# Kernel optimization log

Hardware: AMD Instinct MI355X
Metric: run time of the kernel (lower is better)

## Reference

```python
import jax, jax.numpy as jnp
import numpy as np

EMBED_DIM = 16
HIDDEN = 256
MAX_ORDER = 6
N_EXPERTS = MAX_ORDER + 1
SIZES = [(2 ** (o + 1) + 1) ** 2 for o in range(N_EXPERTS)]  # maze pixels per order
S_MAX = SIZES[-1]  # 16641
D_IN = S_MAX + EMBED_DIM  # padded concat width; embed rows live at [S_MAX:]
BATCH = 1024


def setup_inputs() -> dict:
    key = jax.random.key(0)
    ks = jax.random.split(key, 12)
    w = 0.02  # weight init scale
    return {
        "mazes": jax.random.normal(ks[0], (BATCH, S_MAX), dtype=jnp.float32),
        "orders": jax.random.randint(ks[1], (BATCH,), 0, N_EXPERTS).astype(jnp.int32),
        "embed_table": jax.random.normal(ks[2], (N_EXPERTS, EMBED_DIM), dtype=jnp.float32),
        # per-order input layers, padded to a common [D_IN, 4H]; rows [size_o:S_MAX] unused for order o
        "W_in": jax.random.normal(ks[3], (N_EXPERTS, D_IN, 4 * HIDDEN), dtype=jnp.float32) * w,
        "b_in": jax.random.normal(ks[4], (N_EXPERTS, 4 * HIDDEN), dtype=jnp.float32) * w,
        "W1": jax.random.normal(ks[5], (4 * HIDDEN, 2 * HIDDEN), dtype=jnp.float32) * w,
        "b1": jax.random.normal(ks[6], (2 * HIDDEN,), dtype=jnp.float32) * w,
        "W2": jax.random.normal(ks[7], (2 * HIDDEN, HIDDEN), dtype=jnp.float32) * w,
        "b2": jax.random.normal(ks[8], (HIDDEN,), dtype=jnp.float32) * w,
        "W3": jax.random.normal(ks[9], (HIDDEN, 1), dtype=jnp.float32) * w,
        "b3": jax.random.normal(ks[10], (1,), dtype=jnp.float32) * w,
    }


def reference(mazes, orders, embed_table, W_in, b_in, W1, b1, W2, b2, W3, b3):
    # orders index the embedding table and select the per-order input layer
    e = embed_table[orders]  # [B, E]
    h = jnp.zeros((mazes.shape[0], 4 * HIDDEN), dtype=mazes.dtype)
    # fixed, small loop over experts (structurally distinct weight slices)
    for o in range(N_EXPERTS):
        s = SIZES[o]
        # concat([maze_flat[:s], embed]) exactly as torch.cat([maze_flat, embed])
        x = jnp.concatenate([mazes[:, :s], e], axis=1)  # [B, s+E]
        W = jnp.concatenate([W_in[o, :s], W_in[o, S_MAX:]], axis=0)  # [s+E, 4H]
        y = jax.nn.leaky_relu(x @ W + b_in[o], 0.2)  # [B, 4H]
        h = jnp.where((orders == o)[:, None], y, h)
    z = jax.nn.leaky_relu(h @ W1 + b1, 0.2)
    z = jax.nn.leaky_relu(z @ W2 + b2, 0.2)
    return jax.nn.sigmoid(z @ W3 + b3)  # [B, 1]
```

## Files before the change

kernel.cpp:

```cpp
#include <hip/hip_runtime.h>
#include <cstdint>
#include <cstddef>

#define NEXP 7
#define EMBED_DIM 16
#define FOURH 1024
#define TWOH 512
#define HID 256
#define S_MAX 16641
#define D_IN (S_MAX + EMBED_DIM)
#define BATCH 1024
#define MTILE 192
#define MROWS 384

__constant__ int d_SIZES[NEXP] = {9, 25, 81, 289, 1089, 4225, 16641};
__constant__ int d_KPAD[NEXP] = {64, 64, 128, 320, 1152, 4288, 16704};
__constant__ int d_AOFF[NEXP] = {0, 64, 128, 256, 576, 1728, 6016};
__constant__ int d_KCOFF[NEXP + 1] = {0, 1, 2, 3, 4, 7, 16, 49};

typedef short bf16x8 __attribute__((ext_vector_type(8)));
typedef float f32x4 __attribute__((ext_vector_type(4)));

__device__ __forceinline__ float lrelu(float x) { return x > 0.f ? x : 0.2f * x; }

__device__ __forceinline__ unsigned short f2bf(float x) {
  union { float f; unsigned u; } v;
  v.f = x;
  unsigned r = v.u + 0x7FFFu + ((v.u >> 16) & 1u);
  return (unsigned short)(r >> 16);
}

__global__ __launch_bounds__(1024) void bucket_kernel(
    const int* __restrict__ orders, int* __restrict__ counts,
    int* __restrict__ bases, int* __restrict__ list) {
  __shared__ int c[NEXP], p[NEXP];
  int t = threadIdx.x;
  if (t < NEXP) c[t] = 0;
  __syncthreads();
  int o = orders[t];
  atomicAdd(&c[o], 1);
  __syncthreads();
  if (t == 0) {
    int s = 0;
    for (int i = 0; i < NEXP; ++i) { p[i] = s; s += c[i]; }
  }
  __syncthreads();
  if (t < NEXP) { counts[t] = c[t]; bases[t] = p[t]; }
  __syncthreads();
  int pos = atomicAdd(&p[o], 1);
  list[pos] = t;
}

__global__ __launch_bounds__(1024) void hinit_kernel(
    const float* __restrict__ embed, const float* __restrict__ W_in,
    const float* __restrict__ b_in, float* __restrict__ hinit) {
  int o = blockIdx.x, j = threadIdx.x;
  float a = b_in[o * FOURH + j];
  const float* wr = W_in + (size_t)o * D_IN * FOURH + (size_t)S_MAX * FOURH + j;
#pragma unroll
  for (int e = 0; e < EMBED_DIM; ++e)
    a = fmaf(embed[o * EMBED_DIM + e], wr[(size_t)e * FOURH], a);
  hinit[o * FOURH + j] = a;
}

__global__ __launch_bounds__(256) void hb_kernel(
    const int* __restrict__ orders, const float* __restrict__ hinit,
    float* __restrict__ h) {
  int b = blockIdx.x;
  int o = orders[b];
  const float4* src = (const float4*)(hinit + (size_t)o * FOURH);
  float4* dst = (float4*)(h + (size_t)b * FOURH);
  dst[threadIdx.x] = src[threadIdx.x];
}

__global__ __launch_bounds__(256) void gather_kernel(
    const float* __restrict__ mazes, const int* __restrict__ counts,
    const int* __restrict__ bases, const int* __restrict__ list,
    unsigned short* __restrict__ Ab) {
  int o = blockIdx.x / MROWS;
  int m = blockIdx.x % MROWS;
  int n = counts[o];
  int so = d_SIZES[o];
  int Kp = d_KPAD[o];
  const float* src = nullptr;
  if (m < n) src = mazes + (size_t)list[bases[o] + m] * S_MAX;
  unsigned short* dst = Ab + (size_t)d_AOFF[o] * MROWS + (size_t)m * Kp;
  int nk8 = Kp >> 3;
  for (int k8 = threadIdx.x; k8 < nk8; k8 += 256) {
    int k = k8 * 8;
    union { unsigned short u[8]; uint4 v; } pk;
#pragma unroll
    for (int e = 0; e < 8; ++e) {
      float val = (src && (k + e) < so) ? src[k + e] : 0.f;
      pk.u[e] = f2bf(val);
    }
    *(uint4*)(dst + k) = pk.v;
  }
}

__global__ __launch_bounds__(256, 2) void layerin_mfma(
    const unsigned short* __restrict__ Ab, const float* __restrict__ W_in,
    const int* __restrict__ counts, const int* __restrict__ bases,
    const int* __restrict__ list, float* __restrict__ h) {
  int bx = blockIdx.x;
  int o = 0;
#pragma unroll
  for (int t = 1; t < NEXP; ++t)
    if (bx >= d_KCOFF[t]) o = t;
  int kc = bx - d_KCOFF[o];
  int n = counts[o];
  int m_base = blockIdx.z * MTILE;
  if (m_base >= n) return;

  __shared__ unsigned short sA[8 * 194 * 8];
  __shared__ int sid[MTILE];

  int tid = threadIdx.x;
  int wave = tid >> 6, lane = tid & 63;
  int q = lane >> 4, l16 = lane & 15;

  if (tid < MTILE) sid[tid] = (m_base + tid < n) ? list[bases[o] + m_base + tid] : 0;

  int so = d_SIZES[o];
  int Kp = d_KPAD[o];
  int klo = kc * 512;
  int klen = min(512, Kp - klo);

  int n0 = blockIdx.y * 128 + wave * 32;
  const float* Wc = W_in + (size_t)o * D_IN * FOURH + n0 + l16;
  const unsigned short* Abase =
      Ab + (size_t)d_AOFF[o] * MROWS + (size_t)m_base * Kp + klo;

  f32x4 acc[12][2];
#pragma unroll
  for (int mt = 0; mt < 12; ++mt) {
    acc[mt][0] = (f32x4)0.f;
    acc[mt][1] = (f32x4)0.f;
  }

  int kg = tid & 7;
  int mrow = tid >> 3;

  for (int ks = 0; ks < klen; ks += 64) {
    __syncthreads();
#pragma unroll
    for (int r = 0; r < 6; ++r) {
      int m = r * 32 + mrow;
      uint4 v = *(const uint4*)(Abase + (size_t)m * Kp + ks + kg * 8);
      *(uint4*)&sA[((kg * 194 + m) << 3)] = v;
    }
    __syncthreads();
#pragma unroll
    for (int st = 0; st < 2; ++st) {
      int kb = klo + ks + st * 32 + q * 8;
      bf16x8 bf0, bf1;
#pragma unroll
      for (int j = 0; j < 8; ++j) {
        int kj = kb + j;
        if (kj >= so) kj = so - 1;
        float w0 = Wc[(size_t)kj * FOURH];
        float w1 = Wc[(size_t)kj * FOURH + 16];
        bf0[j] = (short)f2bf(w0);
        bf1[j] = (short)f2bf(w1);
      }
#pragma unroll
      for (int mt = 0; mt < 12; ++mt) {
        bf16x8 af = *(const bf16x8*)&sA[(((st * 4 + q) * 194 + mt * 16 + l16) << 3)];
        acc[mt][0] = __builtin_amdgcn_mfma_f32_16x16x32_bf16(af, bf0, acc[mt][0], 0, 0, 0);
        acc[mt][1] = __builtin_amdgcn_mfma_f32_16x16x32_bf16(af, bf1, acc[mt][1], 0, 0, 0);
      }
    }
  }

  int colA = n0 + l16, colB = n0 + 16 + l16;
#pragma unroll
  for (int mt = 0; mt < 12; ++mt) {
#pragma unroll
    for (int r = 0; r < 4; ++r) {
      int m = mt * 16 + q * 4 + r;
      if (m_base + m < n) {
        int s = sid[m];
        atomicAdd(&h[(size_t)s * FOURH + colA], acc[mt][0][r]);
        atomicAdd(&h[(size_t)s * FOURH + colB], acc[mt][1][r]);
      }
    }
  }
}

template <int KD, int JD, bool ACT_IN>
__global__ __launch_bounds__(256) void mlp_kernel(
    const float* __restrict__ X, const float* __restrict__ W,
    const float* __restrict__ b, float* __restrict__ Y) {
  constexpr int MT2 = 8, KT2 = 256;
  __shared__ float sh[MT2][KT2];
  int tid = threadIdx.x;
  int j = blockIdx.x * 256 + tid;
  int m0 = blockIdx.y * MT2;
  int row = tid >> 5, u = tid & 31;
  const float* xp = X + (size_t)(m0 + row) * KD;
  float acc[MT2];
#pragma unroll
  for (int i = 0; i < MT2; ++i) acc[i] = 0.f;
  for (int kb0 = 0; kb0 < KD; kb0 += KT2) {
    __syncthreads();
#pragma unroll
    for (int c = 0; c < 2; ++c) {
      int kl = c * 128 + u * 4;
      float4 v = *(const float4*)(xp + kb0 + kl);
      if (ACT_IN) {
        v.x = lrelu(v.x); v.y = lrelu(v.y); v.z = lrelu(v.z); v.w = lrelu(v.w);
      }
      *(float4*)&sh[row][kl] = v;
    }
    __syncthreads();
    const float* wb = W + (size_t)kb0 * JD + j;
#pragma unroll 4
    for (int qq = 0; qq < KT2 / 4; ++qq) {
      float w0 = wb[(size_t)(qq * 4 + 0) * JD];
      float w1 = wb[(size_t)(qq * 4 + 1) * JD];
      float w2 = wb[(size_t)(qq * 4 + 2) * JD];
      float w3 = wb[(size_t)(qq * 4 + 3) * JD];
#pragma unroll
      for (int i = 0; i < MT2; ++i) {
        float4 m = *(const float4*)&sh[i][qq * 4];
        acc[i] = fmaf(m.x, w0, acc[i]);
        acc[i] = fmaf(m.y, w1, acc[i]);
        acc[i] = fmaf(m.z, w2, acc[i]);
        acc[i] = fmaf(m.w, w3, acc[i]);
      }
    }
  }
  float bb = b[j];
#pragma unroll
  for (int i = 0; i < MT2; ++i)
    Y[(size_t)(m0 + i) * JD + j] = lrelu(acc[i] + bb);
}

__global__ __launch_bounds__(256) void layer3_kernel(
    const float* __restrict__ z2, const float* __restrict__ W3,
    const float* __restrict__ b3, float* __restrict__ out) {
  int wave = threadIdx.x >> 6, lane = threadIdx.x & 63;
  int b = blockIdx.x * 4 + wave;
  float4 v = *(const float4*)&z2[(size_t)b * HID + lane * 4];
  float4 w = *(const float4*)&W3[lane * 4];
  float d = v.x * w.x + v.y * w.y + v.z * w.z + v.w * w.w;
#pragma unroll
  for (int off = 32; off; off >>= 1) d += __shfl_down(d, off);
  if (lane == 0) out[b] = 1.f / (1.f + expf(-(d + b3[0])));
}

extern "C" void kernel_launch(void* const* d_in, const int* in_sizes, int n_in,
                              void* d_out, int out_size, void* d_ws, size_t ws_size,
                              hipStream_t stream) {
  const float* mazes = (const float*)d_in[0];
  const int* orders = (const int*)d_in[1];
  const float* embed = (const float*)d_in[2];
  const float* W_in = (const float*)d_in[3];
  const float* b_in = (const float*)d_in[4];
  const float* W1 = (const float*)d_in[5];
  const float* b1 = (const float*)d_in[6];
  const float* W2 = (const float*)d_in[7];
  const float* b2 = (const float*)d_in[8];
  const float* W3 = (const float*)d_in[9];
  const float* b3 = (const float*)d_in[10];
  float* out = (float*)d_out;

  char* ws = (char*)d_ws;
  int* counts = (int*)ws;
  int* bases = counts + 8;
  int* list = counts + 16;
  float* hinit = (float*)(ws + 64 * 1024);
  float* h = (float*)(ws + 128 * 1024);
  float* z1 = (float*)(ws + 128 * 1024 + 4 * 1024 * 1024);
  unsigned short* Ab = (unsigned short*)(ws + 128 * 1024 + 8 * 1024 * 1024);
  float* z2 = h;

  bucket_kernel<<<1, 1024, 0, stream>>>(orders, counts, bases, list);
  hinit_kernel<<<NEXP, 1024, 0, stream>>>(embed, W_in, b_in, hinit);
  gather_kernel<<<NEXP * MROWS, 256, 0, stream>>>(mazes, counts, bases, list, Ab);
  hb_kernel<<<BATCH, 256, 0, stream>>>(orders, hinit, h);
  layerin_mfma<<<dim3(49, 8, 2), 256, 0, stream>>>(Ab, W_in, counts, bases, list, h);
  mlp_kernel<FOURH, TWOH, true><<<dim3(2, 128), 256, 0, stream>>>(h, W1, b1, z1);
  mlp_kernel<TWOH, HID, false><<<dim3(1, 128), 256, 0, stream>>>(z1, W2, b2, z2);
  layer3_kernel<<<256, 256, 0, stream>>>(z2, W3, b3, out);
}
```

Before: 804.9 us.

## Fuse small setup kernels and merge layer2 with final layer3 reduction

Merges bucketing and hinit into one prep kernel, folds the per-row h initialisation into the gather kernel, and fuses the second MLP layer with the final dot-product and sigmoid. The first MLP layer now has each thread compute two columns for four rows, using float2 weight loads. The main aim is to cut kernel launches and the z2 round trip through memory. In exchange, layer 2 runs on smaller 4-row tiles, which reuses each weight load less.

```diff
diff --git a/kernel.cpp b/kernel.cpp
--- a/kernel.cpp
+++ b/kernel.cpp
@@ -30,55 +30,55 @@
   return (unsigned short)(r >> 16);
 }
 
-__global__ __launch_bounds__(1024) void bucket_kernel(
+__global__ __launch_bounds__(1024) void prep_kernel(
     const int* __restrict__ orders, int* __restrict__ counts,
-    int* __restrict__ bases, int* __restrict__ list) {
+    int* __restrict__ bases, int* __restrict__ list,
+    const float* __restrict__ embed, const float* __restrict__ W_in,
+    const float* __restrict__ b_in, float* __restrict__ hinit) {
   __shared__ int c[NEXP], p[NEXP];
   int t = threadIdx.x;
-  if (t < NEXP) c[t] = 0;
-  __syncthreads();
-  int o = orders[t];
-  atomicAdd(&c[o], 1);
-  __syncthreads();
-  if (t == 0) {
-    int s = 0;
-    for (int i = 0; i < NEXP; ++i) { p[i] = s; s += c[i]; }
-  }
-  __syncthreads();
-  if (t < NEXP) { counts[t] = c[t]; bases[t] = p[t]; }
-  __syncthreads();
-  int pos = atomicAdd(&p[o], 1);
-  list[pos] = t;
-}
-
-__global__ __launch_bounds__(1024) void hinit_kernel(
-    const float* __restrict__ embed, const float* __restrict__ W_in,
-    const float* __restrict__ b_in, float* __restrict__ hinit) {
-  int o = blockIdx.x, j = threadIdx.x;
-  float a = b_in[o * FOURH + j];
-  const float* wr = W_in + (size_t)o * D_IN * FOURH + (size_t)S_MAX * FOURH + j;
-#pragma unroll
-  for (int e = 0; e < EMBED_DIM; ++e)
-    a = fmaf(embed[o * EMBED_DIM + e], wr[(size_t)e * FOURH], a);
-  hinit[o * FOURH + j] = a;
-}
-
-__global__ __launch_bounds__(256) void hb_kernel(
-    const int* __restrict__ orders, const float* __restrict__ hinit,
-    float* __restrict__ h) {
-  int b = blockIdx.x;
-  int o = orders[b];
-  const float4* src = (const float4*)(hinit + (size_t)o * FOURH);
-  float4* dst = (float4*)(h + (size_t)b * FOURH);
-  dst[threadIdx.x] = src[threadIdx.x];
-}
-
-__global__ __launch_bounds__(256) void gather_kernel(
+  if (blockIdx.x == 0) {
+    if (t < NEXP) c[t] = 0;
+    __syncthreads();
+    int o = orders[t];
+    atomicAdd(&c[o], 1);
+    __syncthreads();
+    if (t == 0) {
+      int s = 0;
+      for (int i = 0; i < NEXP; ++i) { p[i] = s; s += c[i]; }
+    }
+    __syncthreads();
+    if (t < NEXP) { counts[t] = c[t]; bases[t] = p[t]; }
+    __syncthreads();
+    int pos = atomicAdd(&p[o], 1);
+    list[pos] = t;
+  } else {
+    int o = blockIdx.x - 1;
+    float a = b_in[o * FOURH + t];
+    const float* wr = W_in + (size_t)o * D_IN * FOURH + (size_t)S_MAX * FOURH + t;
+#pragma unroll
+    for (int e = 0; e < EMBED_DIM; ++e)
+      a = fmaf(embed[o * EMBED_DIM + e], wr[(size_t)e * FOURH], a);
+    hinit[o * FOURH + t] = a;
+  }
+}
+
+__global__ __launch_bounds__(256) void gather_hb_kernel(
     const float* __restrict__ mazes, const int* __restrict__ counts,
     const int* __restrict__ bases, const int* __restrict__ list,
-    unsigned short* __restrict__ Ab) {
-  int o = blockIdx.x / MROWS;
-  int m = blockIdx.x % MROWS;
+    unsigned short* __restrict__ Ab, const int* __restrict__ orders,
+    const float* __restrict__ hinit, float* __restrict__ h) {
+  int bx = blockIdx.x;
+  if (bx >= NEXP * MROWS) {
+    int b = bx - NEXP * MROWS;
+    int o = orders[b];
+    const float4* src = (const float4*)(hinit + (size_t)o * FOURH);
+    float4* dst = (float4*)(h + (size_t)b * FOURH);
+    dst[threadIdx.x] = src[threadIdx.x];
+    return;
+  }
+  int o = bx / MROWS;
+  int m = bx % MROWS;
   int n = counts[o];
   int so = d_SIZES[o];
   int Kp = d_KPAD[o];
@@ -187,30 +187,78 @@
   }
 }
 
-template <int KD, int JD, bool ACT_IN>
-__global__ __launch_bounds__(256) void mlp_kernel(
+__global__ __launch_bounds__(256) void mlp1_kernel(
     const float* __restrict__ X, const float* __restrict__ W,
     const float* __restrict__ b, float* __restrict__ Y) {
-  constexpr int MT2 = 8, KT2 = 256;
-  __shared__ float sh[MT2][KT2];
+  constexpr int KD = FOURH, JD = TWOH, KT2 = 256;
+  __shared__ float sh[8][KT2];
   int tid = threadIdx.x;
-  int j = blockIdx.x * 256 + tid;
-  int m0 = blockIdx.y * MT2;
-  int row = tid >> 5, u = tid & 31;
-  const float* xp = X + (size_t)(m0 + row) * KD;
-  float acc[MT2];
-#pragma unroll
-  for (int i = 0; i < MT2; ++i) acc[i] = 0.f;
+  int jt = tid & 127, rg = tid >> 7;
+  int j0 = blockIdx.x * 256 + jt * 2;
+  int m0 = blockIdx.y * 8;
+  int srow = tid >> 5, su = tid & 31;
+  const float* xp = X + (size_t)(m0 + srow) * KD;
+  float acc[4][2];
+#pragma unroll
+  for (int i = 0; i < 4; ++i) { acc[i][0] = 0.f; acc[i][1] = 0.f; }
   for (int kb0 = 0; kb0 < KD; kb0 += KT2) {
     __syncthreads();
 #pragma unroll
     for (int c = 0; c < 2; ++c) {
-      int kl = c * 128 + u * 4;
+      int kl = c * 128 + su * 4;
       float4 v = *(const float4*)(xp + kb0 + kl);
-      if (ACT_IN) {
-        v.x = lrelu(v.x); v.y = lrelu(v.y); v.z = lrelu(v.z); v.w = lrelu(v.w);
-      }
-      *(float4*)&sh[row][kl] = v;
+      v.x = lrelu(v.x); v.y = lrelu(v.y); v.z = lrelu(v.z); v.w = lrelu(v.w);
+      *(float4*)&sh[srow][kl] = v;
+    }
+    __syncthreads();
+    const float* wb = W + (size_t)kb0 * JD + j0;
+#pragma unroll 4
+    for (int qq = 0; qq < KT2 / 4; ++qq) {
+      float2 w0 = *(const float2*)(wb + (size_t)(qq * 4 + 0) * JD);
+      float2 w1 = *(const float2*)(wb + (size_t)(qq * 4 + 1) * JD);
+      float2 w2 = *(const float2*)(wb + (size_t)(qq * 4 + 2) * JD);
+      float2 w3 = *(const float2*)(wb + (size_t)(qq * 4 + 3) * JD);
+#pragma unroll
+      for (int i = 0; i < 4; ++i) {
+        float4 m = *(const float4*)&sh[rg * 4 + i][qq * 4];
+        acc[i][0] = fmaf(m.x, w0.x, acc[i][0]);
+        acc[i][0] = fmaf(m.y, w1.x, acc[i][0]);
+        acc[i][0] = fmaf(m.z, w2.x, acc[i][0]);
+        acc[i][0] = fmaf(m.w, w3.x, acc[i][0]);
+        acc[i][1] = fmaf(m.x, w0.y, acc[i][1]);
+        acc[i][1] = fmaf(m.y, w1.y, acc[i][1]);
+        acc[i][1] = fmaf(m.z, w2.y, acc[i][1]);
+        acc[i][1] = fmaf(m.w, w3.y, acc[i][1]);
+      }
+    }
+  }
+  float b0 = b[j0], b1v = b[j0 + 1];
+#pragma unroll
+  for (int i = 0; i < 4; ++i) {
+    size_t row = (size_t)(m0 + rg * 4 + i);
+    Y[row * JD + j0] = lrelu(acc[i][0] + b0);
+    Y[row * JD + j0 + 1] = lrelu(acc[i][1] + b1v);
+  }
+}
+
+__global__ __launch_bounds__(256) void mlp2l3_kernel(
+    const float* __restrict__ X, const float* __restrict__ W,
+    const float* __restrict__ b, const float* __restrict__ W3,
+    const float* __restrict__ b3, float* __restrict__ out) {
+  constexpr int KD = TWOH, JD = HID, KT2 = 256;
+  __shared__ float sh[4][KT2];
+  __shared__ float red[4][4];
+  int tid = threadIdx.x;
+  int j = tid;
+  int m0 = blockIdx.x * 4;
+  int srow = tid >> 6, su = tid & 63;
+  const float* xp = X + (size_t)(m0 + srow) * KD;
+  float acc[4] = {0.f, 0.f, 0.f, 0.f};
+  for (int kb0 = 0; kb0 < KD; kb0 += KT2) {
+    __syncthreads();
+    {
+      float4 v = *(const float4*)(xp + kb0 + su * 4);
+      *(float4*)&sh[srow][su * 4] = v;
     }
     __syncthreads();
     const float* wb = W + (size_t)kb0 * JD + j;
@@ -221,7 +269,7 @@
       float w2 = wb[(size_t)(qq * 4 + 2) * JD];
       float w3 = wb[(size_t)(qq * 4 + 3) * JD];
 #pragma unroll
-      for (int i = 0; i < MT2; ++i) {
+      for (int i = 0; i < 4; ++i) {
         float4 m = *(const float4*)&sh[i][qq * 4];
         acc[i] = fmaf(m.x, w0, acc[i]);
         acc[i] = fmaf(m.y, w1, acc[i]);
@@ -231,22 +279,20 @@
     }
   }
   float bb = b[j];
-#pragma unroll
-  for (int i = 0; i < MT2; ++i)
-    Y[(size_t)(m0 + i) * JD + j] = lrelu(acc[i] + bb);
-}
-
-__global__ __launch_bounds__(256) void layer3_kernel(
-    const float* __restrict__ z2, const float* __restrict__ W3,
-    const float* __restrict__ b3, float* __restrict__ out) {
-  int wave = threadIdx.x >> 6, lane = threadIdx.x & 63;
-  int b = blockIdx.x * 4 + wave;
-  float4 v = *(const float4*)&z2[(size_t)b * HID + lane * 4];
-  float4 w = *(const float4*)&W3[lane * 4];
-  float d = v.x * w.x + v.y * w.y + v.z * w.z + v.w * w.w;
-#pragma unroll
-  for (int off = 32; off; off >>= 1) d += __shfl_down(d, off);
-  if (lane == 0) out[b] = 1.f / (1.f + expf(-(d + b3[0])));
+  float w3j = W3[j];
+  int wave = tid >> 6, lane = tid & 63;
+#pragma unroll
+  for (int i = 0; i < 4; ++i) {
+    float d = lrelu(acc[i] + bb) * w3j;
+#pragma unroll
+    for (int off = 32; off; off >>= 1) d += __shfl_down(d, off);
+    if (lane == 0) red[i][wave] = d;
+  }
+  __syncthreads();
+  if (tid < 4) {
+    float d = red[tid][0] + red[tid][1] + red[tid][2] + red[tid][3];
+    out[m0 + tid] = 1.f / (1.f + expf(-(d + b3[0])));
+  }
 }
 
 extern "C" void kernel_launch(void* const* d_in, const int* in_sizes, int n_in,
@@ -273,14 +319,12 @@
   float* h = (float*)(ws + 128 * 1024);
   float* z1 = (float*)(ws + 128 * 1024 + 4 * 1024 * 1024);
   unsigned short* Ab = (unsigned short*)(ws + 128 * 1024 + 8 * 1024 * 1024);
-  float* z2 = h;
-
-  bucket_kernel<<<1, 1024, 0, stream>>>(orders, counts, bases, list);
-  hinit_kernel<<<NEXP, 1024, 0, stream>>>(embed, W_in, b_in, hinit);
-  gather_kernel<<<NEXP * MROWS, 256, 0, stream>>>(mazes, counts, bases, list, Ab);
-  hb_kernel<<<BATCH, 256, 0, stream>>>(orders, hinit, h);
+
+  prep_kernel<<<1 + NEXP, 1024, 0, stream>>>(orders, counts, bases, list,
+                                             embed, W_in, b_in, hinit);
+  gather_hb_kernel<<<NEXP * MROWS + BATCH, 256, 0, stream>>>(
+      mazes, counts, bases, list, Ab, orders, hinit, h);
   layerin_mfma<<<dim3(49, 8, 2), 256, 0, stream>>>(Ab, W_in, counts, bases, list, h);
-  mlp_kernel<FOURH, TWOH, true><<<dim3(2, 128), 256, 0, stream>>>(h, W1, b1, z1);
-  mlp_kernel<TWOH, HID, false><<<dim3(1, 128), 256, 0, stream>>>(z1, W2, b2, z2);
-  layer3_kernel<<<256, 256, 0, stream>>>(z2, W3, b3, out);
-}
+  mlp1_kernel<<<dim3(2, 128), 256, 0, stream>>>(h, W1, b1, z1);
+  mlp2l3_kernel<<<256, 256, 0, stream>>>(z1, W2, b2, W3, b3, out);
+}
```

Measured after the change: 712.4 us. -11.5%, faster.
